# Kernel tuning notes

Hardware: AMD Instinct MI355X
Metric: run time of the kernel (lower is better)

Reference implementation:

```python
import jax, jax.numpy as jnp
import numpy as np

# static config (matches init_kwargs)
STRIDE, PAD, DIL, DG = 1, 1, 1, 1
KH, KW = 3, 3
CIN, COUT = 64, 64


def setup_inputs() -> dict:
    key = jax.random.key(0)
    k1, k2, k3, k4 = jax.random.split(key, 4)
    N, C, H, W = 4, CIN, 128, 128
    K = KH * KW
    x = jax.random.normal(k1, (N, C, H, W), dtype=jnp.float32)
    offset = jax.random.normal(k2, (N, 2 * DG * K, H, W), dtype=jnp.float32)
    mask = jax.random.uniform(k3, (N, DG * K, H, W), dtype=jnp.float32)
    stdv = 1.0 / np.sqrt(C * K)
    weight = jax.random.uniform(k4, (COUT, C, KH, KW), dtype=jnp.float32,
                                minval=-stdv, maxval=stdv)
    bias = jnp.zeros((COUT,), dtype=jnp.float32)  # no_bias=True -> frozen zeros
    return {"x": x, "offset": offset, "mask": mask, "weight": weight, "bias": bias}


def _dcnv2(x, offset, mask, weight, bias):
    N, C, H, W = x.shape
    Cout, _, kh, kw = weight.shape
    K = kh * kw
    Ho = (H + 2 * PAD - DIL * (kh - 1) - 1) // STRIDE + 1
    Wo = (W + 2 * PAD - DIL * (kw - 1) - 1) // STRIDE + 1
    Cg = C // DG

    # offsets: [N, DG, K, 2(y,x), Ho, Wo]; mask: [N, DG, K, Ho, Wo]
    off = offset.reshape(N, DG, K, 2, Ho, Wo)
    off_y, off_x = off[:, :, :, 0], off[:, :, :, 1]
    m = mask.reshape(N, DG, K, Ho, Wo)

    kidx = jnp.arange(K)
    ky, kx = kidx // kw, kidx % kw
    base_y = (jnp.arange(Ho) * STRIDE - PAD)[None, :] + (ky * DIL)[:, None]  # [K,Ho]
    base_x = (jnp.arange(Wo) * STRIDE - PAD)[None, :] + (kx * DIL)[:, None]  # [K,Wo]

    py = base_y[None, None, :, :, None].astype(x.dtype) + off_y  # [N,DG,K,Ho,Wo]
    px = base_x[None, None, :, None, :].astype(x.dtype) + off_x

    y0 = jnp.floor(py)
    x0 = jnp.floor(px)
    ly = py - y0  # frac weights
    lx = px - x0
    y0i = y0.astype(jnp.int32)
    x0i = x0.astype(jnp.int32)

    xf = x.reshape(N, DG, Cg, H * W)

    def gather(yi, xi):
        # per-corner zero padding (out-of-bounds corners contribute 0)
        valid = ((yi >= 0) & (yi < H) & (xi >= 0) & (xi < W))
        idx = jnp.clip(yi, 0, H - 1) * W + jnp.clip(xi, 0, W - 1)  # [N,DG,K,Ho,Wo]
        idx_b = jnp.broadcast_to(idx[:, :, None], (N, DG, Cg, K, Ho, Wo))
        v = jnp.take_along_axis(xf, idx_b.reshape(N, DG, Cg, -1), axis=3)
        v = v.reshape(N, DG, Cg, K, Ho, Wo)
        return v * valid[:, :, None].astype(x.dtype)

    w00 = ((1 - ly) * (1 - lx))[:, :, None]  # [N,DG,1,K,Ho,Wo]
    w01 = ((1 - ly) * lx)[:, :, None]
    w10 = (ly * (1 - lx))[:, :, None]
    w11 = (ly * lx)[:, :, None]

    val = (gather(y0i, x0i) * w00 + gather(y0i, x0i + 1) * w01
           + gather(y0i + 1, x0i) * w10 + gather(y0i + 1, x0i + 1) * w11)
    cols = val * m[:, :, None]                      # modulation
    cols = cols.reshape(N, C, K, Ho, Wo)            # DG*Cg -> C (contiguous)

    wmat = weight.reshape(Cout, C, K)
    out = jnp.einsum('nckhw,ock->nohw', cols, wmat)
    return out + bias[None, :, None, None]


def reference(x, offset, mask, weight, bias):
    return _dcnv2(x, offset, mask, weight, bias)
```

## Files before the change

### kernel.cpp

```cpp
#include <hip/hip_runtime.h>

#define N_    4
#define C_    64
#define H_    128
#define W_    128
#define KW_   3
#define K_    9
#define COUT_ 64
#define HW_   (H_ * W_)
#define NPIX  (N_ * HW_)
#define KK_   (C_ * K_)

typedef _Float16 h4 __attribute__((ext_vector_type(4)));
typedef _Float16 h8 __attribute__((ext_vector_type(8)));
typedef float v4f __attribute__((ext_vector_type(4)));
typedef int   v4i __attribute__((ext_vector_type(4)));

__global__ __launch_bounds__(256) void prep(
    const float* __restrict__ x, _Float16* __restrict__ xh,
    const float* __restrict__ w, _Float16* __restrict__ wA3)
{
    if (blockIdx.x < 1024) {
        const int n   = blockIdx.x >> 8;
        const int hw0 = (blockIdx.x & 255) * 64;

        __shared__ float tile[64][65];
        const float* xb = x + n * (C_ * HW_);
#pragma unroll
        for (int i = 0; i < 4; ++i) {
            const int idx = i * 256 + threadIdx.x;
            const int q   = idx & 15;
            const int c   = idx >> 4;
            const v4f v = *(const v4f*)&xb[c * HW_ + hw0 + 4 * q];
            tile[4 * q + 0][c] = v.x;
            tile[4 * q + 1][c] = v.y;
            tile[4 * q + 2][c] = v.z;
            tile[4 * q + 3][c] = v.w;
        }
        __syncthreads();
        _Float16* xo = xh + ((size_t)n * HW_ + hw0) * 64;
#pragma unroll
        for (int i = 0; i < 4; ++i) {
            const int idx = i * 256 + threadIdx.x;
            const int c4  = idx & 15;
            const int hr  = idx >> 4;
            h4 v;
            v.x = (_Float16)tile[hr][4 * c4 + 0];
            v.y = (_Float16)tile[hr][4 * c4 + 1];
            v.z = (_Float16)tile[hr][4 * c4 + 2];
            v.w = (_Float16)tile[hr][4 * c4 + 3];
            *(h4*)&xo[hr * 64 + 4 * c4] = v;
        }
    } else {
        const int tid = (blockIdx.x - 1024) * 256 + threadIdx.x;
        if (tid < COUT_ * KK_) {
            const int k   = tid % KK_;
            const int o   = tid / KK_;
            const int c   = k & 63;
            const int tap = k >> 6;
            wA3[tid] = (_Float16)w[o * (C_ * K_) + c * K_ + tap];
        }
    }
}

__global__ __launch_bounds__(256, 4) void dcn_fused(
    const _Float16* __restrict__ xh,
    const float* __restrict__ offset,
    const float* __restrict__ mask,
    const _Float16* __restrict__ wA3,
    const float* __restrict__ bias,
    float* __restrict__ out)
{
    const int tid  = threadIdx.x;
    const int lane = tid & 63;
    const int wv   = tid >> 6;
    const int quad = lane >> 4;
    const int l16  = lane & 15;
    const int g    = lane >> 3;
    const int l8   = lane & 7;

    const int lb  = (blockIdx.x & 7) * 128 + (blockIdx.x >> 3);
    const int pxb = lb * 64;
    const int n   = pxb >> 14;
    const int hwb = pxb & (HW_ - 1);
    const int hww = hwb + wv * 16;

    __shared__ h4  cwh[4][144];
    __shared__ v4i ci[4][144];
    __shared__ _Float16 Bt[4][2][16][72];

#pragma unroll
    for (int r = 0; r < 3; ++r) {
        const int e = r * 64 + lane;
        if (e < 144) {
            const int p  = e / 9;
            const int t  = e - p * 9;
            const int hw = hww + p;
            const int ho = hw >> 7;
            const int wo = hw & (W_ - 1);
            const int ky = t / KW_;
            const int kx = t - ky * KW_;

            const float offy = offset[n * (2 * K_ * HW_) + (2 * t + 0) * HW_ + hw];
            const float offx = offset[n * (2 * K_ * HW_) + (2 * t + 1) * HW_ + hw];
            const float mval = mask[n * (K_ * HW_) + t * HW_ + hw];

            const float py = (float)(ho - 1 + ky) + offy;
            const float qx = (float)(wo - 1 + kx) + offx;
            const float y0f = floorf(py), x0f = floorf(qx);
            const float ly = py - y0f, lx = qx - x0f;
            const int y0 = (int)y0f, x0 = (int)x0f;
            const int y1 = y0 + 1,   x1 = x0 + 1;
            const bool vy0 = (y0 >= 0) & (y0 < H_);
            const bool vy1 = (y1 >= 0) & (y1 < H_);
            const bool vx0 = (x0 >= 0) & (x0 < W_);
            const bool vx1 = (x1 >= 0) & (x1 < W_);
            const int cy0 = min(max(y0, 0), H_ - 1);
            const int cy1 = min(max(y1, 0), H_ - 1);
            const int cx0 = min(max(x0, 0), W_ - 1);
            const int cx1 = min(max(x1, 0), W_ - 1);

            h4 q;
            q.x = (_Float16)((1.f - ly) * (1.f - lx) * mval * ((vy0 && vx0) ? 1.f : 0.f));
            q.y = (_Float16)((1.f - ly) * lx         * mval * ((vy0 && vx1) ? 1.f : 0.f));
            q.z = (_Float16)(ly         * (1.f - lx) * mval * ((vy1 && vx0) ? 1.f : 0.f));
            q.w = (_Float16)(ly         * lx         * mval * ((vy1 && vx1) ? 1.f : 0.f));
            cwh[wv][e] = q;
            v4i ii;
            ii.x = cy0 * W_ + cx0;
            ii.y = cy0 * W_ + cx1;
            ii.z = cy1 * W_ + cx0;
            ii.w = cy1 * W_ + cx1;
            ci[wv][e] = ii;
        }
    }
    __syncthreads();

    const _Float16* xb8 = xh + ((size_t)n * HW_) * 64 + 8 * l8;
    const int pa = g;
    const int pb = g + 8;

    v4f acc[4];
#pragma unroll
    for (int mh = 0; mh < 4; ++mh) acc[mh] = (v4f){0.f, 0.f, 0.f, 0.f};

    h8 LA[2][4], LB[2][4];

#define ISSUE(t, R)                                                         \
    {                                                                       \
        const v4i oa = ci[wv][pa * 9 + (t)];                                \
        const v4i ob = ci[wv][pb * 9 + (t)];                                \
        R[0][0] = *(const h8*)(xb8 + (size_t)oa.x * 64);                    \
        R[0][1] = *(const h8*)(xb8 + (size_t)oa.y * 64);                    \
        R[0][2] = *(const h8*)(xb8 + (size_t)oa.z * 64);                    \
        R[0][3] = *(const h8*)(xb8 + (size_t)oa.w * 64);                    \
        R[1][0] = *(const h8*)(xb8 + (size_t)ob.x * 64);                    \
        R[1][1] = *(const h8*)(xb8 + (size_t)ob.y * 64);                    \
        R[1][2] = *(const h8*)(xb8 + (size_t)ob.z * 64);                    \
        R[1][3] = *(const h8*)(xb8 + (size_t)ob.w * 64);                    \
    }

#define FINISH(t, R, b)                                                     \
    {                                                                       \
        _Pragma("unroll")                                                   \
        for (int h = 0; h < 2; ++h) {                                       \
            const int p = h * 8 + g;                                        \
            const h4 f = cwh[wv][p * 9 + (t)];                              \
            const h8 F0 = {f.x, f.x, f.x, f.x, f.x, f.x, f.x, f.x};         \
            const h8 F1 = {f.y, f.y, f.y, f.y, f.y, f.y, f.y, f.y};         \
            const h8 F2 = {f.z, f.z, f.z, f.z, f.z, f.z, f.z, f.z};         \
            const h8 F3 = {f.w, f.w, f.w, f.w, f.w, f.w, f.w, f.w};         \
            h8 rr = F0 * R[h][0];                                           \
            rr = __builtin_elementwise_fma(F1, R[h][1], rr);                \
            rr = __builtin_elementwise_fma(F2, R[h][2], rr);                \
            rr = __builtin_elementwise_fma(F3, R[h][3], rr);                \
            *(h8*)&Bt[wv][b][p][8 * l8] = rr;                               \
        }                                                                   \
    }

    ISSUE(0, LA)
    ISSUE(1, LB)
    FINISH(0, LA, 0)

#pragma unroll
    for (int t = 0; t < K_; ++t) {
        const int buf = t & 1;
        if ((t & 1) == 0) {
            if (t + 2 < K_) ISSUE(t + 2, LA)
        } else {
            if (t + 2 < K_) ISSUE(t + 2, LB)
        }

#pragma unroll
        for (int kc = 0; kc < 2; ++kc) {
            const h8 bfr = *(const h8*)&Bt[wv][buf][l16][kc * 32 + quad * 8];
#pragma unroll
            for (int mh = 0; mh < 4; ++mh) {
                const h8 afr = *(const h8*)(wA3 + (size_t)(mh * 16 + l16) * KK_
                                            + t * 64 + kc * 32 + quad * 8);
                acc[mh] = __builtin_amdgcn_mfma_f32_16x16x32_f16(
                    afr, bfr, acc[mh], 0, 0, 0);
            }
        }

        if ((t & 1) == 0) {
            if (t + 1 < K_) FINISH(t + 1, LB, buf ^ 1)
        } else {
            if (t + 1 < K_) FINISH(t + 1, LA, buf ^ 1)
        }
    }
#undef ISSUE
#undef FINISH

    float* outb = out + n * (COUT_ * HW_) + hwb + wv * 16 + l16;
#pragma unroll
    for (int mh = 0; mh < 4; ++mh)
#pragma unroll
        for (int r = 0; r < 4; ++r) {
            const int m = mh * 16 + quad * 4 + r;
            outb[m * HW_] = acc[mh][r] + bias[m];
        }
}

__global__ __launch_bounds__(256) void dcn_fallback(
    const float* __restrict__ x, const float* __restrict__ offset,
    const float* __restrict__ mask, const float* __restrict__ wptr,
    const float* __restrict__ bias, float* __restrict__ out)
{
    const int pix = blockIdx.x * 256 + threadIdx.x;
    const int n = pix >> 14, hw = pix & (HW_ - 1);
    const int ho = hw >> 7,  wo = hw & (W_ - 1);
    float acc[COUT_];
#pragma unroll
    for (int o = 0; o < COUT_; ++o) acc[o] = bias[o];
    const float* xn   = x + n * (C_ * HW_);
    const float* offn = offset + n * (2 * K_ * HW_) + hw;
    const float* mn   = mask + n * (K_ * HW_) + hw;
    for (int ct = 0; ct < C_; ct += 8) {
        for (int k = 0; k < K_; ++k) {
            const int ky = k / KW_, kx = k - ky * KW_;
            const float off_y = offn[(2 * k + 0) * HW_];
            const float off_x = offn[(2 * k + 1) * HW_];
            const float m = mn[k * HW_];
            const float py = (float)(ho - 1 + ky) + off_y;
            const float px = (float)(wo - 1 + kx) + off_x;
            const float y0f = floorf(py), x0f = floorf(px);
            const float ly = py - y0f, lx = px - x0f;
            const int y0 = (int)y0f, x0 = (int)x0f, y1 = y0 + 1, x1 = x0 + 1;
            const bool vy0 = (y0 >= 0) & (y0 < H_), vy1 = (y1 >= 0) & (y1 < H_);
            const bool vx0 = (x0 >= 0) & (x0 < W_), vx1 = (x1 >= 0) & (x1 < W_);
            const int cy0 = min(max(y0, 0), H_ - 1), cy1 = min(max(y1, 0), H_ - 1);
            const int cx0 = min(max(x0, 0), W_ - 1), cx1 = min(max(x1, 0), W_ - 1);
            const int i00 = cy0 * W_ + cx0, i01 = cy0 * W_ + cx1;
            const int i10 = cy1 * W_ + cx0, i11 = cy1 * W_ + cx1;
            const float f00 = (1.f - ly) * (1.f - lx) * m * ((vy0 && vx0) ? 1.f : 0.f);
            const float f01 = (1.f - ly) * lx * m * ((vy0 && vx1) ? 1.f : 0.f);
            const float f10 = ly * (1.f - lx) * m * ((vy1 && vx0) ? 1.f : 0.f);
            const float f11 = ly * lx * m * ((vy1 && vx1) ? 1.f : 0.f);
            for (int cc = 0; cc < 8; ++cc) {
                const int c = ct + cc;
                const float* xc = xn + c * HW_;
                const float val = fmaf(f00, xc[i00], fmaf(f01, xc[i01],
                                  fmaf(f10, xc[i10], f11 * xc[i11])));
#pragma unroll
                for (int o = 0; o < COUT_; ++o)
                    acc[o] = fmaf(wptr[o * (C_ * K_) + c * K_ + k], val, acc[o]);
            }
        }
    }
    float* outp = out + n * (COUT_ * HW_) + hw;
#pragma unroll
    for (int o = 0; o < COUT_; ++o) outp[o * HW_] = acc[o];
}

extern "C" void kernel_launch(void* const* d_in, const int* in_sizes, int n_in,
                              void* d_out, int out_size, void* d_ws, size_t ws_size,
                              hipStream_t stream) {
    const float* x      = (const float*)d_in[0];
    const float* offset = (const float*)d_in[1];
    const float* mask   = (const float*)d_in[2];
    const float* weight = (const float*)d_in[3];
    const float* bias   = (const float*)d_in[4];
    float* out = (float*)d_out;

    const size_t xh_bytes = (size_t)NPIX * C_ * sizeof(_Float16);
    const size_t wA_bytes = (size_t)COUT_ * KK_ * sizeof(_Float16);

    if (ws_size >= xh_bytes + wA_bytes) {
        _Float16* xh  = (_Float16*)d_ws;
        _Float16* wA3 = (_Float16*)((char*)d_ws + xh_bytes);
        prep<<<1024 + 144, 256, 0, stream>>>(x, xh, weight, wA3);
        dcn_fused<<<NPIX / 64, 256, 0, stream>>>(xh, offset, mask, wA3, bias, out);
    } else {
        dcn_fallback<<<NPIX / 256, 256, 0, stream>>>(x, offset, mask, weight, bias, out);
    }
}
```

Measured before the change: 123.9 us.

## Build MFMA B fragments in registers and pre-swizzle weights into fragment order

Each lane now gathers the four bilinear corners for its own pixel (l16) and channel slices (quad*8 and quad*8+32), then combines them directly into the MFMA B operand in registers. This removes the LDS staging buffer Bt and its write/read round trip. The weight matrix is reordered in prep so each A fragment is one contiguous 512-element block, which makes the per-lane loads coalesced. Scheduling barriers and s_setprio are added around the MFMA phase, and the occupancy hint drops from 4 to 3 waves per SIMD to make room for the larger register prefetch buffers.

```diff
diff --git a/kernel.cpp b/kernel.cpp
--- a/kernel.cpp
+++ b/kernel.cpp
@@ -18,7 +18,7 @@
 
 __global__ __launch_bounds__(256) void prep(
     const float* __restrict__ x, _Float16* __restrict__ xh,
-    const float* __restrict__ w, _Float16* __restrict__ wA3)
+    const float* __restrict__ w, _Float16* __restrict__ wA4)
 {
     if (blockIdx.x < 1024) {
         const int n   = blockIdx.x >> 8;
@@ -54,20 +54,25 @@
     } else {
         const int tid = (blockIdx.x - 1024) * 256 + threadIdx.x;
         if (tid < COUT_ * KK_) {
-            const int k   = tid % KK_;
-            const int o   = tid / KK_;
-            const int c   = k & 63;
-            const int tap = k >> 6;
-            wA3[tid] = (_Float16)w[o * (C_ * K_) + c * K_ + tap];
-        }
-    }
-}
-
-__global__ __launch_bounds__(256, 4) void dcn_fused(
+            const int blk = tid >> 9;
+            const int r   = tid & 511;
+            const int l16 = r >> 5;
+            const int ch  = r & 31;
+            const int t   = blk >> 3;
+            const int kc  = (blk >> 2) & 1;
+            const int mh  = blk & 3;
+            const int o   = mh * 16 + l16;
+            const int c   = kc * 32 + ch;
+            wA4[tid] = (_Float16)w[o * (C_ * K_) + c * K_ + t];
+        }
+    }
+}
+
+__global__ __launch_bounds__(256, 3) void dcn_fused(
     const _Float16* __restrict__ xh,
     const float* __restrict__ offset,
     const float* __restrict__ mask,
-    const _Float16* __restrict__ wA3,
+    const _Float16* __restrict__ wA4,
     const float* __restrict__ bias,
     float* __restrict__ out)
 {
@@ -76,8 +81,6 @@
     const int wv   = tid >> 6;
     const int quad = lane >> 4;
     const int l16  = lane & 15;
-    const int g    = lane >> 3;
-    const int l8   = lane & 7;
 
     const int lb  = (blockIdx.x & 7) * 128 + (blockIdx.x >> 3);
     const int pxb = lb * 64;
@@ -87,7 +90,6 @@
 
     __shared__ h4  cwh[4][144];
     __shared__ v4i ci[4][144];
-    __shared__ _Float16 Bt[4][2][16][72];
 
 #pragma unroll
     for (int r = 0; r < 3; ++r) {
@@ -136,81 +138,77 @@
     }
     __syncthreads();
 
-    const _Float16* xb8 = xh + ((size_t)n * HW_) * 64 + 8 * l8;
-    const int pa = g;
-    const int pb = g + 8;
+    const _Float16* xbq = xh + ((size_t)n * HW_) * 64 + quad * 8;
 
     v4f acc[4];
 #pragma unroll
     for (int mh = 0; mh < 4; ++mh) acc[mh] = (v4f){0.f, 0.f, 0.f, 0.f};
 
-    h8 LA[2][4], LB[2][4];
+    h8 LA[4][2], LB[4][2];
 
 #define ISSUE(t, R)                                                         \
     {                                                                       \
-        const v4i oa = ci[wv][pa * 9 + (t)];                                \
-        const v4i ob = ci[wv][pb * 9 + (t)];                                \
-        R[0][0] = *(const h8*)(xb8 + (size_t)oa.x * 64);                    \
-        R[0][1] = *(const h8*)(xb8 + (size_t)oa.y * 64);                    \
-        R[0][2] = *(const h8*)(xb8 + (size_t)oa.z * 64);                    \
-        R[0][3] = *(const h8*)(xb8 + (size_t)oa.w * 64);                    \
-        R[1][0] = *(const h8*)(xb8 + (size_t)ob.x * 64);                    \
-        R[1][1] = *(const h8*)(xb8 + (size_t)ob.y * 64);                    \
-        R[1][2] = *(const h8*)(xb8 + (size_t)ob.z * 64);                    \
-        R[1][3] = *(const h8*)(xb8 + (size_t)ob.w * 64);                    \
-    }
-
-#define FINISH(t, R, b)                                                     \
+        const v4i o = ci[wv][l16 * 9 + (t)];                                \
+        const _Float16* a0 = xbq + (size_t)o.x * 64;                        \
+        const _Float16* a1 = xbq + (size_t)o.y * 64;                        \
+        const _Float16* a2 = xbq + (size_t)o.z * 64;                        \
+        const _Float16* a3 = xbq + (size_t)o.w * 64;                        \
+        R[0][0] = *(const h8*)(a0);  R[0][1] = *(const h8*)(a0 + 32);       \
+        R[1][0] = *(const h8*)(a1);  R[1][1] = *(const h8*)(a1 + 32);       \
+        R[2][0] = *(const h8*)(a2);  R[2][1] = *(const h8*)(a2 + 32);       \
+        R[3][0] = *(const h8*)(a3);  R[3][1] = *(const h8*)(a3 + 32);       \
+    }
+
+#define COMBINE(t, R, bfr0, bfr1)                                           \
     {                                                                       \
-        _Pragma("unroll")                                                   \
-        for (int h = 0; h < 2; ++h) {                                       \
-            const int p = h * 8 + g;                                        \
-            const h4 f = cwh[wv][p * 9 + (t)];                              \
-            const h8 F0 = {f.x, f.x, f.x, f.x, f.x, f.x, f.x, f.x};         \
-            const h8 F1 = {f.y, f.y, f.y, f.y, f.y, f.y, f.y, f.y};         \
-            const h8 F2 = {f.z, f.z, f.z, f.z, f.z, f.z, f.z, f.z};         \
-            const h8 F3 = {f.w, f.w, f.w, f.w, f.w, f.w, f.w, f.w};         \
-            h8 rr = F0 * R[h][0];                                           \
-            rr = __builtin_elementwise_fma(F1, R[h][1], rr);                \
-            rr = __builtin_elementwise_fma(F2, R[h][2], rr);                \
-            rr = __builtin_elementwise_fma(F3, R[h][3], rr);                \
-            *(h8*)&Bt[wv][b][p][8 * l8] = rr;                               \
-        }                                                                   \
+        const h4 f = cwh[wv][l16 * 9 + (t)];                                \
+        const h8 F0 = {f.x, f.x, f.x, f.x, f.x, f.x, f.x, f.x};             \
+        const h8 F1 = {f.y, f.y, f.y, f.y, f.y, f.y, f.y, f.y};             \
+        const h8 F2 = {f.z, f.z, f.z, f.z, f.z, f.z, f.z, f.z};             \
+        const h8 F3 = {f.w, f.w, f.w, f.w, f.w, f.w, f.w, f.w};             \
+        bfr0 = F0 * R[0][0];                                                \
+        bfr0 = __builtin_elementwise_fma(F1, R[1][0], bfr0);                \
+        bfr0 = __builtin_elementwise_fma(F2, R[2][0], bfr0);                \
+        bfr0 = __builtin_elementwise_fma(F3, R[3][0], bfr0);                \
+        bfr1 = F0 * R[0][1];                                                \
+        bfr1 = __builtin_elementwise_fma(F1, R[1][1], bfr1);                \
+        bfr1 = __builtin_elementwise_fma(F2, R[2][1], bfr1);                \
+        bfr1 = __builtin_elementwise_fma(F3, R[3][1], bfr1);                \
     }
 
     ISSUE(0, LA)
     ISSUE(1, LB)
-    FINISH(0, LA, 0)
+    __builtin_amdgcn_sched_barrier(0);
+
+    const _Float16* ab = wA4 + l16 * 32 + quad * 8;
 
 #pragma unroll
     for (int t = 0; t < K_; ++t) {
-        const int buf = t & 1;
+        h8 bfr0, bfr1;
         if ((t & 1) == 0) {
+            COMBINE(t, LA, bfr0, bfr1)
             if (t + 2 < K_) ISSUE(t + 2, LA)
         } else {
+            COMBINE(t, LB, bfr0, bfr1)
             if (t + 2 < K_) ISSUE(t + 2, LB)
         }
-
+        __builtin_amdgcn_sched_barrier(0);
+
+        __builtin_amdgcn_s_setprio(1);
 #pragma unroll
         for (int kc = 0; kc < 2; ++kc) {
-            const h8 bfr = *(const h8*)&Bt[wv][buf][l16][kc * 32 + quad * 8];
+            const h8 bb = kc ? bfr1 : bfr0;
 #pragma unroll
             for (int mh = 0; mh < 4; ++mh) {
-                const h8 afr = *(const h8*)(wA3 + (size_t)(mh * 16 + l16) * KK_
-                                            + t * 64 + kc * 32 + quad * 8);
+                const h8 afr = *(const h8*)(ab + (size_t)(t * 8 + kc * 4 + mh) * 512);
                 acc[mh] = __builtin_amdgcn_mfma_f32_16x16x32_f16(
-                    afr, bfr, acc[mh], 0, 0, 0);
+                    afr, bb, acc[mh], 0, 0, 0);
             }
         }
-
-        if ((t & 1) == 0) {
-            if (t + 1 < K_) FINISH(t + 1, LB, buf ^ 1)
-        } else {
-            if (t + 1 < K_) FINISH(t + 1, LA, buf ^ 1)
-        }
+        __builtin_amdgcn_s_setprio(0);
     }
 #undef ISSUE
-#undef FINISH
+#undef COMBINE
 
     float* outb = out + n * (COUT_ * HW_) + hwb + wv * 16 + l16;
 #pragma unroll
@@ -288,9 +286,9 @@
 
     if (ws_size >= xh_bytes + wA_bytes) {
         _Float16* xh  = (_Float16*)d_ws;
-        _Float16* wA3 = (_Float16*)((char*)d_ws + xh_bytes);
-        prep<<<1024 + 144, 256, 0, stream>>>(x, xh, weight, wA3);
-        dcn_fused<<<NPIX / 64, 256, 0, stream>>>(xh, offset, mask, wA3, bias, out);
+        _Float16* wA4 = (_Float16*)((char*)d_ws + xh_bytes);
+        prep<<<1024 + 144, 256, 0, stream>>>(x, xh, weight, wA4);
+        dcn_fused<<<NPIX / 64, 256, 0, stream>>>(xh, offset, mask, wA4, bias, out);
     } else {
         dcn_fallback<<<NPIX / 256, 256, 0, stream>>>(x, offset, mask, weight, bias, out);
     }
```

Result: slower. 130.4 us (+5.2%).
